# Performance work log

Measured on AMD Instinct MI355X. Metric: run time of the kernel, lower is better.

The kernel has to match this reference:

```python
import jax, jax.numpy as jnp
import numpy as np

D_MODEL = 1024
N_HEADS = 16
D_HEAD = D_MODEL // N_HEADS


def setup_inputs() -> dict:
    key = jax.random.key(0)
    k_x, k_wqkv, k_bqkv, k_wo, k_bo = jax.random.split(key, 5)
    B, S = 2, 2048
    x = jax.random.normal(k_x, (B, S, D_MODEL), dtype=jnp.float32)
    # torch Linear: y = x @ W.T + b; store W as [out, in] like torch
    bound1 = 1.0 / np.sqrt(D_MODEL)
    W_qkv = jax.random.uniform(k_wqkv, (3 * D_MODEL, D_MODEL), minval=-bound1, maxval=bound1, dtype=jnp.float32)
    b_qkv = jax.random.uniform(k_bqkv, (3 * D_MODEL,), minval=-bound1, maxval=bound1, dtype=jnp.float32)
    W_out = jax.random.uniform(k_wo, (D_MODEL, D_MODEL), minval=-bound1, maxval=bound1, dtype=jnp.float32)
    b_out = jax.random.uniform(k_bo, (D_MODEL,), minval=-bound1, maxval=bound1, dtype=jnp.float32)
    return {"x": x, "W_qkv": W_qkv, "b_qkv": b_qkv, "W_out": W_out, "b_out": b_out}


def reference(x, W_qkv, b_qkv, W_out, b_out):
    B, S, D = x.shape
    qkv = x @ W_qkv.T + b_qkv                       # [B, S, 3D]
    qkv = qkv.reshape(B, S, 3, N_HEADS, D_HEAD)
    qkv = jnp.transpose(qkv, (2, 0, 3, 1, 4))       # [3, B, H, S, Dh]
    q, k, v = qkv[0], qkv[1], qkv[2]
    scores = jnp.einsum('bhqd,bhkd->bhqk', q, k) / np.sqrt(D_HEAD).astype(np.float32)
    causal = jnp.tril(jnp.ones((S, S), dtype=bool))
    scores = jnp.where(causal[None, None], scores, jnp.float32(-jnp.inf))
    attn = jax.nn.softmax(scores, axis=-1)          # dropout p=0 -> identity
    out = jnp.einsum('bhqk,bhkd->bhqd', attn, v)    # [B, H, S, Dh]
    out = jnp.transpose(out, (0, 2, 1, 3)).reshape(B, S, D)
    return out @ W_out.T + b_out
```

## Files before the change

### kernel.cpp

```cpp
#include <hip/hip_runtime.h>
#include <hip/hip_bf16.h>
#include <cstdint>


#define DEV __device__ __forceinline__

#define VT_STRIDE 2048

using bf16x8 = __attribute__((ext_vector_type(8))) short;
using f32x4  = __attribute__((ext_vector_type(4))) float;
using f32x16 = __attribute__((ext_vector_type(16))) float;
using u32x4  = __attribute__((ext_vector_type(4))) unsigned;

DEV unsigned short f2bf(float f) {
  unsigned u = __builtin_bit_cast(unsigned, f);
  u = (u + 0x7fffu + ((u >> 16) & 1u)) >> 16;
  return (unsigned short)u;
}

typedef __attribute__((address_space(1))) unsigned int as1_uint;
typedef __attribute__((address_space(3))) unsigned int as3_uint;

DEV void gload_lds16(const void* g, void* l) {
  __builtin_amdgcn_global_load_lds(
      (as1_uint*)(uintptr_t)g,
      (as3_uint*)(unsigned int)(uintptr_t)l,
      16, 0, 0);
}

#define N4_X  (4096 * 1024 / 4)
#define N4_WQ (3072 * 1024 / 4)
#define N4_WO (1024 * 1024 / 4)
__global__ __launch_bounds__(256) void cvt_all_k(const float* __restrict__ x,
                                                 const float* __restrict__ wq,
                                                 const float* __restrict__ wo,
                                                 unsigned short* __restrict__ xb,
                                                 unsigned short* __restrict__ wqb,
                                                 unsigned short* __restrict__ wob) {
  int i = blockIdx.x * 256 + threadIdx.x;
  const float* in; unsigned short* out;
  if (i < N4_X)                { in = x;  out = xb; }
  else if (i < N4_X + N4_WQ)   { i -= N4_X;  in = wq; out = wqb; }
  else                         { i -= N4_X + N4_WQ; in = wo; out = wob; }
  float4 v = reinterpret_cast<const float4*>(in)[i];
  ushort4 o;
  o.x = f2bf(v.x); o.y = f2bf(v.y); o.z = f2bf(v.z); o.w = f2bf(v.w);
  reinterpret_cast<ushort4*>(out)[i] = o;
}

__global__ __launch_bounds__(256) void transpose_v_k(const unsigned short* __restrict__ V,
                                                     unsigned short* __restrict__ Vt) {
  const int bh = blockIdx.x;
  const int st = blockIdx.y;
  const int tid = threadIdx.x;
  __shared__ unsigned short T[64 * 64];
  const unsigned short* src = V + ((size_t)bh * 2048 + st * 64) * 64;

#pragma unroll
  for (int it = 0; it < 2; ++it) {
    const int c = it * 256 + tid;
    const int L = c * 16;
    const int S = L ^ (((L >> 10) & 7) << 4);
    gload_lds16((const char*)src + S, (char*)T + L);
  }
  __syncthreads();

#pragma unroll
  for (int it = 0; it < 2; ++it) {
    const int c = it * 256 + tid;
    const int d = c >> 3;
    const int s_off = (c & 7) * 8;
    const int xg = (c & 7) << 4;
    bf16x8 pk;
#pragma unroll
    for (int j = 0; j < 8; ++j)
      pk[j] = *(const short*)((const char*)T + (((s_off + j) * 128 + d * 2) ^ xg));
    *(bf16x8*)(Vt + (size_t)(bh * 64 + d) * VT_STRIDE + st * 64 + s_off) = pk;
  }
}

template <int MODE, int N, int K>
__global__ __launch_bounds__(256) void gemm_bt(const unsigned short* __restrict__ A,
                                               const unsigned short* __restrict__ W,
                                               const float* __restrict__ bias,
                                               float* __restrict__ Cout,
                                               unsigned short* __restrict__ Qp,
                                               unsigned short* __restrict__ Kp,
                                               unsigned short* __restrict__ Vp) {
  __shared__ unsigned short As[2][128 * 64];
  __shared__ unsigned short Bs[2][128 * 64];
  const int tid = threadIdx.x;
  const int m0 = blockIdx.x * 128;
  const int n0 = blockIdx.y * 128;
  const int w = tid >> 6, lane = tid & 63, g = lane >> 4, lr = lane & 15;
  const int wr = w >> 1, wc = w & 1;
  const int xr = (lr & 7) << 4;

  f32x4 acc[4][4];
#pragma unroll
  for (int i = 0; i < 4; ++i)
#pragma unroll
    for (int j = 0; j < 4; ++j)
#pragma unroll
      for (int r = 0; r < 4; ++r) acc[i][j][r] = 0.f;

#define GSTAGE(buf, kt)                                                                     \
  do {                                                                                      \
    _Pragma("unroll")                                                                       \
    for (int it = 0; it < 4; ++it) {                                                        \
      const int c = it * 256 + tid;                                                         \
      const int row = c >> 3;                                                               \
      const int colb = ((c & 7) * 16) ^ ((row & 7) << 4);                                   \
      gload_lds16((const char*)(A + (size_t)(m0 + row) * K + (kt)) + colb,                  \
                  (char*)As[buf] + c * 16);                                                 \
      gload_lds16((const char*)(W + (size_t)(n0 + row) * K + (kt)) + colb,                  \
                  (char*)Bs[buf] + c * 16);                                                 \
    }                                                                                       \
  } while (0)

  GSTAGE(0, 0);
  int cur = 0;
  const int nsteps = K / 64;
  for (int step = 0; step < nsteps; ++step) {
    if (step + 1 < nsteps) {
      GSTAGE(cur ^ 1, (step + 1) * 64);
      asm volatile("s_waitcnt vmcnt(8)" ::: "memory");
    } else {
      asm volatile("s_waitcnt vmcnt(0)" ::: "memory");
    }
    __builtin_amdgcn_s_barrier();
    __builtin_amdgcn_sched_barrier(0);

    const char* AsC = (const char*)As[cur];
    const char* BsC = (const char*)Bs[cur];
    __builtin_amdgcn_s_setprio(1);
#pragma unroll
    for (int ks = 0; ks < 2; ++ks) {
      bf16x8 af[4], bf[4];
#pragma unroll
      for (int mi = 0; mi < 4; ++mi)
        af[mi] = *(const bf16x8*)(AsC +
                   ((((wr * 64 + mi * 16 + lr) * 128) + ks * 64 + g * 16) ^ xr));
#pragma unroll
      for (int ni = 0; ni < 4; ++ni)
        bf[ni] = *(const bf16x8*)(BsC +
                   ((((wc * 64 + ni * 16 + lr) * 128) + ks * 64 + g * 16) ^ xr));
#pragma unroll
      for (int mi = 0; mi < 4; ++mi)
#pragma unroll
        for (int ni = 0; ni < 4; ++ni)
          acc[mi][ni] = __builtin_amdgcn_mfma_f32_16x16x32_bf16(af[mi], bf[ni], acc[mi][ni], 0, 0, 0);
    }
    __builtin_amdgcn_s_setprio(0);

    asm volatile("" ::: "memory");
    __builtin_amdgcn_s_barrier();
    __builtin_amdgcn_sched_barrier(0);
    cur ^= 1;
  }
#undef GSTAGE

  if (MODE == 0) {
#pragma unroll
    for (int ni = 0; ni < 4; ++ni) {
      const int col = n0 + wc * 64 + ni * 16 + lr;
      const float bv = bias[col];
#pragma unroll
      for (int mi = 0; mi < 4; ++mi)
#pragma unroll
        for (int r = 0; r < 4; ++r) {
          const int row = m0 + wr * 64 + mi * 16 + g * 4 + r;
          Cout[(size_t)row * N + col] = acc[mi][ni][r] + bv;
        }
    }
  } else {
#pragma unroll
    for (int ni = 0; ni < 4; ++ni) {
      const int col = n0 + wc * 64 + ni * 16 + lr;
      const float bv = bias[col];
      const int which = col >> 10;
      const int h = (col >> 6) & 15;
      const int d = col & 63;
      unsigned short* P = which == 0 ? Qp : which == 1 ? Kp : Vp;
#pragma unroll
      for (int mi = 0; mi < 4; ++mi)
#pragma unroll
        for (int r = 0; r < 4; ++r) {
          const int row = m0 + wr * 64 + mi * 16 + g * 4 + r;
          const int b = row >> 11, s = row & 2047;
          P[(((size_t)(b * 16 + h) * 2048 + s) << 6) + d] = f2bf(acc[mi][ni][r] + bv);
        }
    }
  }
}

__global__ __launch_bounds__(256) void attn_fwd(const unsigned short* __restrict__ Q,
                                                const unsigned short* __restrict__ Kg,
                                                const unsigned short* __restrict__ Vt,
                                                unsigned short* __restrict__ AO) {
  const int bh = blockIdx.x;
  const int y  = blockIdx.y;
  const int qt = (y < 8) ? (15 - y) : (y - 8);
  const int tid = threadIdx.x;
  const int w = tid >> 6, lane = tid & 63;
  const int l31 = lane & 31, hi = lane >> 5;
  const int xr = (lane & 7) << 4;
  const unsigned short* Qp = Q  + (size_t)bh * 2048 * 64;
  const unsigned short* Kp = Kg + (size_t)bh * 2048 * 64;
  const unsigned short* Vp = Vt + (size_t)bh * 64 * VT_STRIDE;
  const int b = bh >> 4, h = bh & 15;

  __shared__ unsigned short Ks[2][64 * 64];
  __shared__ unsigned short Vs[2][64 * 64];

  const float C = 0.1803368801f;

  const int L0 = tid * 16,         L1 = (tid + 256) * 16;
  const int G0 = L0 ^ (((L0 >> 7) & 7) << 4);
  const int G1 = L1 ^ (((L1 >> 7) & 7) << 4);

#define STAGE(buf, kvb)                                                                     \
  do {                                                                                      \
    gload_lds16((const char*)Kp + (size_t)(kvb) * 128 + G0, (char*)Ks[buf] + L0);           \
    gload_lds16((const char*)Kp + (size_t)(kvb) * 128 + G1, (char*)Ks[buf] + L1);           \
    gload_lds16((const char*)Vp + (size_t)(G0 >> 7) * (VT_STRIDE * 2) + (size_t)(kvb) * 2 + \
                    (G0 & 127), (char*)Vs[buf] + L0);                                       \
    gload_lds16((const char*)Vp + (size_t)(G1 >> 7) * (VT_STRIDE * 2) + (size_t)(kvb) * 2 + \
                    (G1 & 127), (char*)Vs[buf] + L1);                                       \
  } while (0)

  const int nb = 2 * qt + 2;
  const int qrow0 = qt * 128 + w * 32;

  STAGE(0, 0);
  int cur = 0;

  bf16x8 qf[4];
#pragma unroll
  for (int ds = 0; ds < 4; ++ds)
    qf[ds] = *(const bf16x8*)(Qp + (size_t)(qrow0 + l31) * 64 + ds * 16 + hi * 8);

  f32x16 o0, o1;
#pragma unroll
  for (int r = 0; r < 16; ++r) { o0[r] = 0.f; o1[r] = 0.f; }
  float lp = 0.f;

  for (int t = 0; t < nb; ++t) {
    const int kvb = t * 64;
    if (t + 1 < nb) {
      STAGE(cur ^ 1, (t + 1) * 64);
      asm volatile("s_waitcnt vmcnt(4)" ::: "memory");
    } else {
      asm volatile("s_waitcnt vmcnt(0)" ::: "memory");
    }
    __builtin_amdgcn_s_barrier();
    __builtin_amdgcn_sched_barrier(0);

    const char* KsC = (const char*)Ks[cur];
    const char* VsC = (const char*)Vs[cur];

    f32x16 s0, s1;
#pragma unroll
    for (int r = 0; r < 16; ++r) { s0[r] = 0.f; s1[r] = 0.f; }
    __builtin_amdgcn_s_setprio(1);
#pragma unroll
    for (int ds = 0; ds < 4; ++ds) {
      bf16x8 k0 = *(const bf16x8*)(KsC + ((l31 * 128 + ds * 32 + hi * 16) ^ xr));
      bf16x8 k1 = *(const bf16x8*)(KsC + (((32 + l31) * 128 + ds * 32 + hi * 16) ^ xr));
      s0 = __builtin_amdgcn_mfma_f32_32x32x16_bf16(k0, qf[ds], s0, 0, 0, 0);
      s1 = __builtin_amdgcn_mfma_f32_32x32x16_bf16(k1, qf[ds], s1, 0, 0, 0);
    }
    __builtin_amdgcn_s_setprio(0);

    if (t >= nb - 2) {
      const int thr = qrow0 + l31 - kvb;
#pragma unroll
      for (int reg = 0; reg < 16; ++reg) {
        const int koff = (reg & 3) + 8 * (reg >> 2) + 4 * hi;
        if (koff > thr)      s0[reg] = -INFINITY;
        if (koff + 32 > thr) s1[reg] = -INFINITY;
      }
    }

#pragma unroll
    for (int reg = 0; reg < 16; ++reg) {
      float a0 = exp2f(s0[reg] * C);
      float a1 = exp2f(s1[reg] * C);
      s0[reg] = a0; s1[reg] = a1;
      lp += a0 + a1;
    }

    bf16x8 pa[4];
#pragma unroll
    for (int kb = 0; kb < 2; ++kb) {
      unsigned wv[8], tv[8];
#pragma unroll
      for (int j = 0; j < 8; ++j) {
        float e0 = kb ? s1[2 * j] : s0[2 * j];
        float e1 = kb ? s1[2 * j + 1] : s0[2 * j + 1];
        asm("v_cvt_pk_bf16_f32 %0, %1, %2" : "=v"(wv[j]) : "v"(e0), "v"(e1));
      }
#pragma unroll
      for (int j = 0; j < 8; ++j) tv[j] = (unsigned)__shfl_xor((int)wv[j], 32);
      u32x4 ua, ub;
      ua[0] = hi ? tv[2] : wv[0]; ua[1] = hi ? tv[3] : wv[1];
      ua[2] = hi ? wv[2] : tv[0]; ua[3] = hi ? wv[3] : tv[1];
      ub[0] = hi ? tv[6] : wv[4]; ub[1] = hi ? tv[7] : wv[5];
      ub[2] = hi ? wv[6] : tv[4]; ub[3] = hi ? wv[7] : tv[5];
      pa[kb * 2]     = __builtin_bit_cast(bf16x8, ua);
      pa[kb * 2 + 1] = __builtin_bit_cast(bf16x8, ub);
    }

    __builtin_amdgcn_s_setprio(1);
#pragma unroll
    for (int ks = 0; ks < 4; ++ks) {
      bf16x8 v0 = *(const bf16x8*)(VsC + ((l31 * 128 + ks * 32 + hi * 16) ^ xr));
      bf16x8 v1 = *(const bf16x8*)(VsC + (((32 + l31) * 128 + ks * 32 + hi * 16) ^ xr));
      o0 = __builtin_amdgcn_mfma_f32_32x32x16_bf16(pa[ks], v0, o0, 0, 0, 0);
      o1 = __builtin_amdgcn_mfma_f32_32x32x16_bf16(pa[ks], v1, o1, 0, 0, 0);
    }
    __builtin_amdgcn_s_setprio(0);

    asm volatile("" ::: "memory");
    __builtin_amdgcn_s_barrier();
    __builtin_amdgcn_sched_barrier(0);
    cur ^= 1;
  }

  lp += __shfl_xor(lp, 32);
  const float inv = 1.0f / lp;
#pragma unroll
  for (int reg = 0; reg < 16; ++reg) {
    const int qoff = (reg & 3) + 8 * (reg >> 2) + 4 * hi;
    const float li = __shfl(inv, qoff);
    const int row = qrow0 + qoff;
    AO[(size_t)(b * 2048 + row) * 1024 + h * 64 + l31]      = f2bf(o0[reg] * li);
    AO[(size_t)(b * 2048 + row) * 1024 + h * 64 + 32 + l31] = f2bf(o1[reg] * li);
  }
}

extern "C" void kernel_launch(void* const* d_in, const int* in_sizes, int n_in,
                              void* d_out, int out_size, void* d_ws, size_t ws_size,
                              hipStream_t stream) {
  const float* x     = (const float*)d_in[0];
  const float* W_qkv = (const float*)d_in[1];
  const float* b_qkv = (const float*)d_in[2];
  const float* W_out = (const float*)d_in[3];
  const float* b_out = (const float*)d_in[4];
  float* out = (float*)d_out;

  char* ws = (char*)d_ws;
  unsigned short* xb  = (unsigned short*)(ws);
  unsigned short* AOb = (unsigned short*)(ws);
  unsigned short* wqb = (unsigned short*)(ws + ((size_t)8 << 20));
  unsigned short* wob = (unsigned short*)(ws + ((size_t)14 << 20));
  unsigned short* Qb  = (unsigned short*)(ws + ((size_t)16 << 20));
  unsigned short* Kb  = (unsigned short*)(ws + ((size_t)24 << 20));
  unsigned short* Vb  = (unsigned short*)(ws + ((size_t)32 << 20));
  unsigned short* Vtb = (unsigned short*)(ws + ((size_t)40 << 20));

  cvt_all_k<<<(N4_X + N4_WQ + N4_WO) / 256, 256, 0, stream>>>(x, W_qkv, W_out, xb, wqb, wob);

  gemm_bt<1, 3072, 1024><<<dim3(32, 24), 256, 0, stream>>>(xb, wqb, b_qkv, nullptr, Qb, Kb, Vb);
  transpose_v_k<<<dim3(32, 32), 256, 0, stream>>>(Vb, Vtb);
  attn_fwd<<<dim3(32, 16), 256, 0, stream>>>(Qb, Kb, Vtb, AOb);
  gemm_bt<0, 1024, 1024><<<dim3(32, 8), 256, 0, stream>>>(AOb, wob, b_out, out, nullptr, nullptr, nullptr);
}
```

Baseline: 123.7 us.

## Halve attention block size to 64 query rows and fold softmax scale into Q

The attention kernel now runs 128-thread blocks of two waves covering 64 query rows, launched on a 32x32 grid in descending tile order instead of 256-thread blocks over 128 rows. Each block loads the same 64-row K/V tiles from LDS but shares them across fewer waves, and only the last KV block needs causal masking. The softmax scale (log2e/sqrt(d)) is folded into Q when the QKV GEMM writes it, and exp2 uses the raw v_exp_f32 instruction. The aim is finer causal load balancing, more resident blocks, and fewer multiplies in the softmax loop. The cost is extra K/V staging traffic per query row, plus a slight precision change from scaling Q before bf16 rounding.

Measured after the change: 116.4 us. 1.06x faster.

```diff
diff --git a/kernel.cpp b/kernel.cpp
--- a/kernel.cpp
+++ b/kernel.cpp
@@ -6,6 +6,7 @@
 #define DEV __device__ __forceinline__
 
 #define VT_STRIDE 2048
+#define QSCALE 0.1803368801f
 
 using bf16x8 = __attribute__((ext_vector_type(8))) short;
 using f32x4  = __attribute__((ext_vector_type(4))) float;
@@ -16,6 +17,12 @@
   unsigned u = __builtin_bit_cast(unsigned, f);
   u = (u + 0x7fffu + ((u >> 16) & 1u)) >> 16;
   return (unsigned short)u;
+}
+
+DEV float exp2_hw(float x) {
+  float r;
+  asm("v_exp_f32 %0, %1" : "=v"(r) : "v"(x));
+  return r;
 }
 
 typedef __attribute__((address_space(1))) unsigned int as1_uint;
@@ -182,25 +189,25 @@
       const int h = (col >> 6) & 15;
       const int d = col & 63;
       unsigned short* P = which == 0 ? Qp : which == 1 ? Kp : Vp;
+      const float scl = which == 0 ? QSCALE : 1.0f;
 #pragma unroll
       for (int mi = 0; mi < 4; ++mi)
 #pragma unroll
         for (int r = 0; r < 4; ++r) {
           const int row = m0 + wr * 64 + mi * 16 + g * 4 + r;
           const int b = row >> 11, s = row & 2047;
-          P[(((size_t)(b * 16 + h) * 2048 + s) << 6) + d] = f2bf(acc[mi][ni][r] + bv);
+          P[(((size_t)(b * 16 + h) * 2048 + s) << 6) + d] = f2bf((acc[mi][ni][r] + bv) * scl);
         }
     }
   }
 }
 
-__global__ __launch_bounds__(256) void attn_fwd(const unsigned short* __restrict__ Q,
+__global__ __launch_bounds__(128) void attn_fwd(const unsigned short* __restrict__ Q,
                                                 const unsigned short* __restrict__ Kg,
                                                 const unsigned short* __restrict__ Vt,
                                                 unsigned short* __restrict__ AO) {
   const int bh = blockIdx.x;
-  const int y  = blockIdx.y;
-  const int qt = (y < 8) ? (15 - y) : (y - 8);
+  const int qt = 31 - blockIdx.y;
   const int tid = threadIdx.x;
   const int w = tid >> 6, lane = tid & 63;
   const int l31 = lane & 31, hi = lane >> 5;
@@ -213,24 +220,20 @@
   __shared__ unsigned short Ks[2][64 * 64];
   __shared__ unsigned short Vs[2][64 * 64];
 
-  const float C = 0.1803368801f;
-
-  const int L0 = tid * 16,         L1 = (tid + 256) * 16;
-  const int G0 = L0 ^ (((L0 >> 7) & 7) << 4);
-  const int G1 = L1 ^ (((L1 >> 7) & 7) << 4);
-
 #define STAGE(buf, kvb)                                                                     \
   do {                                                                                      \
-    gload_lds16((const char*)Kp + (size_t)(kvb) * 128 + G0, (char*)Ks[buf] + L0);           \
-    gload_lds16((const char*)Kp + (size_t)(kvb) * 128 + G1, (char*)Ks[buf] + L1);           \
-    gload_lds16((const char*)Vp + (size_t)(G0 >> 7) * (VT_STRIDE * 2) + (size_t)(kvb) * 2 + \
-                    (G0 & 127), (char*)Vs[buf] + L0);                                       \
-    gload_lds16((const char*)Vp + (size_t)(G1 >> 7) * (VT_STRIDE * 2) + (size_t)(kvb) * 2 + \
-                    (G1 & 127), (char*)Vs[buf] + L1);                                       \
+    _Pragma("unroll")                                                                       \
+    for (int it = 0; it < 4; ++it) {                                                        \
+      const int Lc = (it * 128 + tid) * 16;                                                 \
+      const int Gc = Lc ^ (((Lc >> 7) & 7) << 4);                                           \
+      gload_lds16((const char*)Kp + (size_t)(kvb) * 128 + Gc, (char*)Ks[buf] + Lc);         \
+      gload_lds16((const char*)Vp + (size_t)(Gc >> 7) * (VT_STRIDE * 2) +                   \
+                      (size_t)(kvb) * 2 + (Gc & 127), (char*)Vs[buf] + Lc);                 \
+    }                                                                                       \
   } while (0)
 
-  const int nb = 2 * qt + 2;
-  const int qrow0 = qt * 128 + w * 32;
+  const int nb = qt + 1;
+  const int qrow0 = qt * 64 + w * 32;
 
   STAGE(0, 0);
   int cur = 0;
@@ -249,7 +252,7 @@
     const int kvb = t * 64;
     if (t + 1 < nb) {
       STAGE(cur ^ 1, (t + 1) * 64);
-      asm volatile("s_waitcnt vmcnt(4)" ::: "memory");
+      asm volatile("s_waitcnt vmcnt(8)" ::: "memory");
     } else {
       asm volatile("s_waitcnt vmcnt(0)" ::: "memory");
     }
@@ -272,8 +275,8 @@
     }
     __builtin_amdgcn_s_setprio(0);
 
-    if (t >= nb - 2) {
-      const int thr = qrow0 + l31 - kvb;
+    if (t == nb - 1) {
+      const int thr = w * 32 + l31;
 #pragma unroll
       for (int reg = 0; reg < 16; ++reg) {
         const int koff = (reg & 3) + 8 * (reg >> 2) + 4 * hi;
@@ -284,8 +287,8 @@
 
 #pragma unroll
     for (int reg = 0; reg < 16; ++reg) {
-      float a0 = exp2f(s0[reg] * C);
-      float a1 = exp2f(s1[reg] * C);
+      float a0 = exp2_hw(s0[reg]);
+      float a1 = exp2_hw(s1[reg]);
       s0[reg] = a0; s1[reg] = a1;
       lp += a0 + a1;
     }
@@ -337,6 +340,7 @@
     AO[(size_t)(b * 2048 + row) * 1024 + h * 64 + l31]      = f2bf(o0[reg] * li);
     AO[(size_t)(b * 2048 + row) * 1024 + h * 64 + 32 + l31] = f2bf(o1[reg] * li);
   }
+#undef STAGE
 }
 
 extern "C" void kernel_launch(void* const* d_in, const int* in_sizes, int n_in,
@@ -363,6 +367,6 @@
 
   gemm_bt<1, 3072, 1024><<<dim3(32, 24), 256, 0, stream>>>(xb, wqb, b_qkv, nullptr, Qb, Kb, Vb);
   transpose_v_k<<<dim3(32, 32), 256, 0, stream>>>(Vb, Vtb);
-  attn_fwd<<<dim3(32, 16), 256, 0, stream>>>(Qb, Kb, Vtb, AOb);
+  attn_fwd<<<dim3(32, 32), 128, 0, stream>>>(Qb, Kb, Vtb, AOb);
   gemm_bt<0, 1024, 1024><<<dim3(32, 8), 256, 0, stream>>>(AOb, wob, b_out, out, nullptr, nullptr, nullptr);
 }
```
